# Kernel optimization log

Measured on AMD Instinct MI355X. Metric: run time of the kernel, lower is better.

The kernel has to match this reference:

```python
import jax, jax.numpy as jnp
import numpy as np

H, I_, N, K, R, NL = 768, 1536, 16, 4, 48, 8
B, L, DIN = 4, 1024, 13
DA, RP = 128, 4
EPS = 1e-5

def _rmsnorm(x, w):
    v = jnp.mean(jnp.square(x), axis=-1, keepdims=True)
    return x * jax.lax.rsqrt(v + EPS) * w

def _causal_dwconv(hs, w, b):
    # hs: [B, I, L]; w: [I, K] depthwise kernel; causal (left) padding = K-1
    out = jax.lax.conv_general_dilated(
        hs, w[:, None, :], window_strides=(1,), padding=[(K - 1, 0)],
        dimension_numbers=('NCH', 'OIH', 'NCH'), feature_group_count=hs.shape[1])
    return out + b[None, :, None]

def _selective_scan(u, dt, Bm, Cm, A, D):
    # u, dt: [B, L, I]; Bm, Cm: [B, L, N]; A: [I, N]; D: [I]
    def step(h, inp):
        dt_t, B_t, C_t, u_t = inp          # [B,I], [B,N], [B,N], [B,I]
        dA = jnp.exp(dt_t[:, :, None] * A)  # [B,I,N]
        h = dA * h + (dt_t * u_t)[:, :, None] * B_t[:, None, :]
        y = jnp.einsum('bin,bn->bi', h, C_t)
        return h, y
    h0 = jnp.zeros((u.shape[0], A.shape[0], A.shape[1]), u.dtype)
    xs = (jnp.swapaxes(dt, 0, 1), jnp.swapaxes(Bm, 0, 1),
          jnp.swapaxes(Cm, 0, 1), jnp.swapaxes(u, 0, 1))
    _, ys = jax.lax.scan(step, h0, xs)
    return jnp.swapaxes(ys, 0, 1) + u * D

def _mamba_block(x, norm_w, in_w, conv_w, conv_b, xproj_w, dt_w, dt_b, A_log, D, out_w):
    res = x
    h = _rmsnorm(x, norm_w)
    proj = h @ in_w.T                      # [B,L,2I]
    hs, gate = jnp.split(proj, 2, axis=-1)
    hs = jnp.swapaxes(hs, 1, 2)            # [B,I,L]
    hs = jax.nn.silu(_causal_dwconv(hs, conv_w, conv_b))
    u = jnp.swapaxes(hs, 1, 2)             # [B,L,I]
    ssm = u @ xproj_w.T                    # [B,L,R+2N]
    ts, Bm, Cm = ssm[..., :R], ssm[..., R:R + N], ssm[..., R + N:]
    dt = jax.nn.softplus(ts @ dt_w.T + dt_b)
    y = _selective_scan(u, dt, Bm, Cm, -jnp.exp(A_log), D)
    y = y * jax.nn.silu(gate)
    return res + y @ out_w.T

def _forward(x, mlp_in_w1, mlp_in_b1, mlp_in_w2, mlp_in_b2, mlp_in_w3, mlp_in_b3,
             layers_norm_w, layers_in_proj_w, layers_conv_w, layers_conv_b,
             layers_x_proj_w, layers_dt_w, layers_dt_b, layers_A_log, layers_D,
             layers_out_proj_w, norm_f_w, attn_ws1, attn_ws2,
             mlp_out_w1, mlp_out_b1, mlp_out_w2, mlp_out_b2, mlp_out_w3, mlp_out_b3):
    h = jax.nn.relu(x @ mlp_in_w1.T + mlp_in_b1)
    h = jax.nn.relu(h @ mlp_in_w2.T + mlp_in_b2)
    h = h @ mlp_in_w3.T + mlp_in_b3        # [B,L,H]
    for l in range(NL):
        h = _mamba_block(h, layers_norm_w[l], layers_in_proj_w[l], layers_conv_w[l],
                         layers_conv_b[l], layers_x_proj_w[l], layers_dt_w[l],
                         layers_dt_b[l], layers_A_log[l], layers_D[l],
                         layers_out_proj_w[l])
    h = _rmsnorm(h, norm_f_w)              # final norm_f
    # attention pooling: softmax over the sequence dim (dim=1)
    attn = jax.nn.softmax(jnp.tanh(h @ attn_ws1.T) @ attn_ws2.T, axis=1)  # [B,L,r]
    m = jnp.einsum('blr,blh->brh', attn, h)  # bmm(attn^T, h) -> [B,r,H]
    flat = m.reshape(m.shape[0], -1)         # [B, r*H]
    o = jax.nn.relu(flat @ mlp_out_w1.T + mlp_out_b1)
    o = jax.nn.relu(o @ mlp_out_w2.T + mlp_out_b2)
    return o @ mlp_out_w3.T + mlp_out_b3     # [B,1]

def setup_inputs():
    key = jax.random.key(0)
    ks = iter(jax.random.split(key, 40))
    def nrm(shape, s=0.02):
        return jax.random.normal(next(ks), shape, dtype=jnp.float32) * s
    A_log = jnp.log(jnp.tile(jnp.arange(1, N + 1, dtype=jnp.float32)[None, None, :], (NL, I_, 1)))
    return {
        'x': jax.random.normal(next(ks), (B, L, DIN), dtype=jnp.float32),
        'mlp_in_w1': nrm((256, DIN)), 'mlp_in_b1': jnp.zeros((256,), jnp.float32),
        'mlp_in_w2': nrm((256, 256)), 'mlp_in_b2': jnp.zeros((256,), jnp.float32),
        'mlp_in_w3': nrm((H, 256)), 'mlp_in_b3': jnp.zeros((H,), jnp.float32),
        'layers_norm_w': jnp.ones((NL, H), jnp.float32),
        'layers_in_proj_w': nrm((NL, 2 * I_, H)),
        'layers_conv_w': nrm((NL, I_, K), 0.1),
        'layers_conv_b': jnp.zeros((NL, I_), jnp.float32),
        'layers_x_proj_w': nrm((NL, R + 2 * N, I_)),
        'layers_dt_w': nrm((NL, I_, R)),
        'layers_dt_b': jnp.full((NL, I_), -4.6, jnp.float32),
        'layers_A_log': A_log,
        'layers_D': jnp.ones((NL, I_), jnp.float32),
        'layers_out_proj_w': nrm((NL, H, I_)),
        'norm_f_w': jnp.ones((H,), jnp.float32),
        'attn_ws1': nrm((DA, H)), 'attn_ws2': nrm((RP, DA)),
        'mlp_out_w1': nrm((256, H * RP)), 'mlp_out_b1': jnp.zeros((256,), jnp.float32),
        'mlp_out_w2': nrm((256, 256)), 'mlp_out_b2': jnp.zeros((256,), jnp.float32),
        'mlp_out_w3': nrm((1, 256)), 'mlp_out_b3': jnp.zeros((1,), jnp.float32),
    }

def reference(x, mlp_in_w1, mlp_in_b1, mlp_in_w2, mlp_in_b2, mlp_in_w3, mlp_in_b3,
              layers_norm_w, layers_in_proj_w, layers_conv_w, layers_conv_b,
              layers_x_proj_w, layers_dt_w, layers_dt_b, layers_A_log, layers_D,
              layers_out_proj_w, norm_f_w, attn_ws1, attn_ws2,
              mlp_out_w1, mlp_out_b1, mlp_out_w2, mlp_out_b2, mlp_out_w3, mlp_out_b3):
    return _forward(x, mlp_in_w1, mlp_in_b1, mlp_in_w2, mlp_in_b2, mlp_in_w3, mlp_in_b3,
                    layers_norm_w, layers_in_proj_w, layers_conv_w, layers_conv_b,
                    layers_x_proj_w, layers_dt_w, layers_dt_b, layers_A_log, layers_D,
                    layers_out_proj_w, norm_f_w, attn_ws1, attn_ws2,
                    mlp_out_w1, mlp_out_b1, mlp_out_w2, mlp_out_b2, mlp_out_w3, mlp_out_b3)
```

## Files before the change

### kernel.cpp

```cpp
#include <hip/hip_runtime.h>
#include <cstddef>
#include <cstdint>

#define HD    768
#define ID    1536
#define ND    16
#define KD    4
#define RD    48
#define NLAY  8
#define BB    4
#define LL    1024
#define BL    4096
#define DIN   13
#define DA_   128
#define RP_   4

#define NC    32
#define CS    32

typedef _Float16 f16;
typedef f16 f16x8 __attribute__((ext_vector_type(8)));
typedef float f32x4 __attribute__((ext_vector_type(4)));

__device__ __forceinline__ float softplus_f(float x) {
    return (x > 20.f) ? x : log1pf(expf(x));
}

__device__ __forceinline__ float fast_exp2(float x) {
#if __has_builtin(__builtin_amdgcn_exp2f)
    return __builtin_amdgcn_exp2f(x);
#else
    return exp2f(x);
#endif
}

__global__ __launch_bounds__(256) void cast_f16_k(
    const float* __restrict__ in, f16* __restrict__ out, int n)
{
    int i = (blockIdx.x * 256 + threadIdx.x) * 4;
    if (i + 3 < n) {
        float4 v = *(const float4*)(in + i);
        out[i]     = (f16)v.x;
        out[i + 1] = (f16)v.y;
        out[i + 2] = (f16)v.z;
        out[i + 3] = (f16)v.w;
    } else {
        for (int j = i; j < n; ++j) out[j] = (f16)in[j];
    }
}

__global__ __launch_bounds__(256) void cast_dtw_k(
    const float* __restrict__ in, f16* __restrict__ out)
{
    int idx = blockIdx.x * 256 + threadIdx.x;
    if (idx >= NLAY * ID * 64) return;
    int k = idx & 63, r = idx >> 6;
    out[idx] = (k < RD) ? (f16)in[r * RD + k] : (f16)0.f;
}

__global__ __launch_bounds__(256) void zero_k(float* __restrict__ p, int n)
{
    int i = blockIdx.x * 256 + threadIdx.x;
    if (i < n) p[i] = 0.f;
}

__device__ __forceinline__ void epilogue_store(
    float v, int row, int col, int N,
    const float* __restrict__ res, int ldres,
    float* __restrict__ C, int ldc,
    f16* __restrict__ Cb, int ldcb, int ncb, int act,
    const float* __restrict__ bias)
{
    if (col >= N) return;
    if (bias) v += bias[col];
    if (act == 1) v = fmaxf(v, 0.f);
    else if (act == 2) v = tanhf(v);
    else if (act == 3) v = softplus_f(v);
    if (res) v += res[(size_t)row * ldres + col];
    if (C) C[(size_t)row * ldc + col] = v;
    if (Cb && col < ncb) Cb[(size_t)row * ldcb + col] = (f16)v;
}

__device__ __forceinline__ void async_copy16(const f16* g, f16* l) {
    __builtin_amdgcn_global_load_lds(
        (const __attribute__((address_space(1))) void*)g,
        (__attribute__((address_space(3))) void*)l, 16, 0, 0);
}

__global__ __launch_bounds__(256) void hgemm_k(
    const f16* __restrict__ A, int lda,
    const f16* __restrict__ W, int ldw,
    const float* __restrict__ bias,
    const float* __restrict__ res, int ldres,
    float* __restrict__ C, int ldc,
    f16* __restrict__ Cb, int ldcb, int ncb,
    int M, int N, int K, int act)
{
    __shared__ f16 As[128 * 32];
    __shared__ f16 Bs[128 * 32];
    int tid = threadIdx.x;
    int wave = tid >> 6, lane = tid & 63;
    int m0 = blockIdx.y * 128, n0 = blockIdx.x * 128;

    int wm = wave & 1, wn = wave >> 1;
    int lm = lane & 15;
    int kq = (lane >> 4) * 8;

    int srow = lane >> 2;
    int skc  = (lane & 3) * 8;

    f32x4 acc[4][4] = {};

    for (int k0 = 0; k0 < K; k0 += 32) {
#pragma unroll
        for (int it = 0; it < 2; ++it) {
            int c16 = wave + it * 4;
            int row = c16 * 16 + srow;
            const f16* ga = A + (size_t)(m0 + row) * lda + k0 + skc;
            const f16* gb = W + (size_t)(n0 + row) * ldw + k0 + skc;
            async_copy16(ga, As + c16 * 512);
            async_copy16(gb, Bs + c16 * 512);
        }
        __syncthreads();

        f16x8 af[4], bf[4];
#pragma unroll
        for (int mt = 0; mt < 4; ++mt)
            af[mt] = *(const f16x8*)(As + (wm * 64 + mt * 16 + lm) * 32 + kq);
#pragma unroll
        for (int nt = 0; nt < 4; ++nt)
            bf[nt] = *(const f16x8*)(Bs + (wn * 64 + nt * 16 + lm) * 32 + kq);
#pragma unroll
        for (int mt = 0; mt < 4; ++mt)
#pragma unroll
            for (int nt = 0; nt < 4; ++nt)
                acc[mt][nt] = __builtin_amdgcn_mfma_f32_16x16x32_f16(
                    af[mt], bf[nt], acc[mt][nt], 0, 0, 0);
        __syncthreads();
    }

    int rq = (lane >> 4) * 4;
#pragma unroll
    for (int mt = 0; mt < 4; ++mt)
#pragma unroll
        for (int nt = 0; nt < 4; ++nt) {
            int col = n0 + wn * 64 + nt * 16 + lm;
#pragma unroll
            for (int r = 0; r < 4; ++r) {
                int row = m0 + wm * 64 + mt * 16 + rq + r;
                epilogue_store(acc[mt][nt][r], row, col, N, res, ldres,
                               C, ldc, Cb, ldcb, ncb, act, bias);
            }
        }
}

__global__ __launch_bounds__(256) void hgemm64_k(
    const f16* __restrict__ A, int lda,
    const f16* __restrict__ W, int ldw,
    const float* __restrict__ bias,
    const float* __restrict__ res, int ldres,
    float* __restrict__ C, int ldc,
    f16* __restrict__ Cb, int ldcb, int ncb,
    int M, int N, int K, int act)
{
    __shared__ f16 As[64 * 32];
    __shared__ f16 Bs[64 * 32];
    int tid = threadIdx.x;
    int wave = tid >> 6, lane = tid & 63;
    int m0 = blockIdx.y * 64, n0 = blockIdx.x * 64;

    int wm = wave & 1, wn = wave >> 1;
    int lm = lane & 15;
    int kq = (lane >> 4) * 8;

    int srow = tid >> 2;
    int skc  = (tid & 3) * 8;

    f32x4 acc[2][2] = {};

    for (int k0 = 0; k0 < K; k0 += 32) {
        const f16* ga = A + (size_t)(m0 + srow) * lda + k0 + skc;
        const f16* gb = W + (size_t)(n0 + srow) * ldw + k0 + skc;
        async_copy16(ga, As + wave * 512);
        async_copy16(gb, Bs + wave * 512);
        __syncthreads();

        f16x8 af[2], bf[2];
#pragma unroll
        for (int mt = 0; mt < 2; ++mt)
            af[mt] = *(const f16x8*)(As + (wm * 32 + mt * 16 + lm) * 32 + kq);
#pragma unroll
        for (int nt = 0; nt < 2; ++nt)
            bf[nt] = *(const f16x8*)(Bs + (wn * 32 + nt * 16 + lm) * 32 + kq);
#pragma unroll
        for (int mt = 0; mt < 2; ++mt)
#pragma unroll
            for (int nt = 0; nt < 2; ++nt)
                acc[mt][nt] = __builtin_amdgcn_mfma_f32_16x16x32_f16(
                    af[mt], bf[nt], acc[mt][nt], 0, 0, 0);
        __syncthreads();
    }

    int rq = (lane >> 4) * 4;
#pragma unroll
    for (int mt = 0; mt < 2; ++mt)
#pragma unroll
        for (int nt = 0; nt < 2; ++nt) {
            int col = n0 + wn * 32 + nt * 16 + lm;
#pragma unroll
            for (int r = 0; r < 4; ++r) {
                int row = m0 + wm * 32 + mt * 16 + rq + r;
                epilogue_store(acc[mt][nt][r], row, col, N, res, ldres,
                               C, ldc, Cb, ldcb, ncb, act, bias);
            }
        }
}

#define BM 64
#define BN 64
#define BKK 16
__global__ __launch_bounds__(256) void gemm_k(
    const float* __restrict__ A, int lda,
    const float* __restrict__ W,
    const float* __restrict__ bias,
    float* __restrict__ C, int ldc,
    f16* __restrict__ Cb, int ldcb,
    int M, int N, int K, int act)
{
    __shared__ float As[BKK][BM + 4];
    __shared__ float Ws[BKK][BN + 4];
    int tid = threadIdx.x;
    int tx = tid & 15, ty = tid >> 4;
    int m0 = blockIdx.y * BM, n0 = blockIdx.x * BN;
    float acc[4][4] = {};
    int arow = tid >> 2;
    int acol = (tid & 3) * 4;

    for (int k0 = 0; k0 < K; k0 += BKK) {
        int gm = m0 + arow;
        int gn = n0 + arow;
#pragma unroll
        for (int j = 0; j < 4; ++j) {
            int gk = k0 + acol + j;
            float av = 0.f, wv = 0.f;
            if (gm < M && gk < K) av = A[(size_t)gm * lda + gk];
            if (gn < N && gk < K) wv = W[(size_t)gn * K + gk];
            As[acol + j][arow] = av;
            Ws[acol + j][arow] = wv;
        }
        __syncthreads();
#pragma unroll
        for (int k = 0; k < BKK; ++k) {
            float a[4], b[4];
#pragma unroll
            for (int i = 0; i < 4; ++i) a[i] = As[k][ty * 4 + i];
#pragma unroll
            for (int j = 0; j < 4; ++j) b[j] = Ws[k][tx * 4 + j];
#pragma unroll
            for (int i = 0; i < 4; ++i)
#pragma unroll
                for (int j = 0; j < 4; ++j)
                    acc[i][j] += a[i] * b[j];
        }
        __syncthreads();
    }

#pragma unroll
    for (int i = 0; i < 4; ++i) {
        int row = m0 + ty * 4 + i;
        if (row >= M) continue;
#pragma unroll
        for (int j = 0; j < 4; ++j) {
            int col = n0 + tx * 4 + j;
            if (col >= N) continue;
            float v = acc[i][j];
            if (bias) v += bias[col];
            if (act == 1) v = fmaxf(v, 0.f);
            if (C) C[(size_t)row * ldc + col] = v;
            if (Cb) Cb[(size_t)row * ldcb + col] = (f16)v;
        }
    }
}

__global__ __launch_bounds__(256) void rmsnorm_k(
    const float* __restrict__ x, const float* __restrict__ w,
    f16* __restrict__ out)
{
    int row = blockIdx.x;
    const float* xr = x + (size_t)row * HD;
    int tid = threadIdx.x;
    float v0 = xr[tid], v1 = xr[tid + 256], v2 = xr[tid + 512];
    __shared__ float red[256];
    red[tid] = v0 * v0 + v1 * v1 + v2 * v2;
    __syncthreads();
    for (int o = 128; o; o >>= 1) {
        if (tid < o) red[tid] += red[tid + o];
        __syncthreads();
    }
    float scale = rsqrtf(red[0] / (float)HD + 1e-5f);
    f16* outr = out + (size_t)row * HD;
    outr[tid]       = (f16)(v0 * scale * w[tid]);
    outr[tid + 256] = (f16)(v1 * scale * w[tid + 256]);
    outr[tid + 512] = (f16)(v2 * scale * w[tid + 512]);
}

__global__ __launch_bounds__(256) void conv_silu_k(
    const f16* __restrict__ projb, const float* __restrict__ cw,
    const float* __restrict__ cb, f16* __restrict__ ub)
{
    int idx = blockIdx.x * 256 + threadIdx.x;
    if (idx >= BL * (ID / 8)) return;
    int i8  = (idx % (ID / 8)) * 8;
    int row = idx / (ID / 8);
    int t = row & (LL - 1);

    float4 wv[8];
#pragma unroll
    for (int j = 0; j < 8; ++j)
        wv[j] = *(const float4*)(cw + (i8 + j) * KD);

    float s[8];
    float4 cb0 = *(const float4*)(cb + i8);
    float4 cb1 = *(const float4*)(cb + i8 + 4);
    s[0] = cb0.x; s[1] = cb0.y; s[2] = cb0.z; s[3] = cb0.w;
    s[4] = cb1.x; s[5] = cb1.y; s[6] = cb1.z; s[7] = cb1.w;

#pragma unroll
    for (int k = 0; k < KD; ++k) {
        int tt = t - (KD - 1) + k;
        if (tt < 0) continue;
        f16x8 p = *(const f16x8*)(projb + (size_t)(row - (KD - 1) + k) * (2 * ID) + i8);
#pragma unroll
        for (int j = 0; j < 8; ++j) {
            float wk = (k == 0) ? wv[j].x : (k == 1) ? wv[j].y
                     : (k == 2) ? wv[j].z : wv[j].w;
            s[j] += (float)p[j] * wk;
        }
    }
    f16x8 o;
#pragma unroll
    for (int j = 0; j < 8; ++j) {
        float v = s[j] / (1.f + expf(-s[j]));
        o[j] = (f16)v;
    }
    *(f16x8*)(ub + (size_t)row * ID + i8) = o;
}

__global__ __launch_bounds__(256) void scan1_k(
    const f16*   __restrict__ dtf,
    const float* __restrict__ ssm,
    const f16*   __restrict__ ub,
    const float* __restrict__ A_log,
    float* __restrict__ Pw, float* __restrict__ Hw)
{
    int b = blockIdx.z, c = blockIdx.y;
    int i = blockIdx.x * 256 + threadIdx.x;
    __shared__ float sB[CS * 16];
    for (int idx = threadIdx.x; idx < CS * 16; idx += 256) {
        int t = idx >> 4, n = idx & 15;
        sB[idx] = ssm[((size_t)(b * LL + c * CS + t)) * 80 + 48 + n];
    }
    __syncthreads();

    float Ain[16];
#pragma unroll
    for (int n = 0; n < 16; ++n)
        Ain[n] = -expf(A_log[i * ND + n]) * 1.44269504f;

    float h[16];
    float sdt = 0.f;
#pragma unroll
    for (int n = 0; n < 16; ++n) h[n] = 0.f;

    for (int t = 0; t < CS; ++t) {
        size_t row = (size_t)(b * LL + c * CS + t);
        float dtv = (float)dtf[row * ID + i];
        float x = dtv * (float)ub[row * ID + i];
        sdt += dtv;
        const float4* Bv = (const float4*)(sB + t * 16);
        float4 B0 = Bv[0], B1 = Bv[1], B2 = Bv[2], B3 = Bv[3];
        float Bf[16] = {B0.x, B0.y, B0.z, B0.w, B1.x, B1.y, B1.z, B1.w,
                        B2.x, B2.y, B2.z, B2.w, B3.x, B3.y, B3.z, B3.w};
#pragma unroll
        for (int n = 0; n < 16; ++n) {
            float dA = fast_exp2(dtv * Ain[n]);
            h[n] = dA * h[n] + x * Bf[n];
        }
    }
    size_t off = (((size_t)(b * NC + c) * ID + i) << 4);
    float4* pw = (float4*)(Pw + off);
    float4* hw = (float4*)(Hw + off);
#pragma unroll
    for (int q = 0; q < 4; ++q) {
        pw[q] = make_float4(fast_exp2(sdt * Ain[q*4]),
                            fast_exp2(sdt * Ain[q*4+1]),
                            fast_exp2(sdt * Ain[q*4+2]),
                            fast_exp2(sdt * Ain[q*4+3]));
        hw[q] = make_float4(h[q*4], h[q*4+1], h[q*4+2], h[q*4+3]);
    }
}

__global__ __launch_bounds__(256) void scan_comb_k(
    const float* __restrict__ Pw, float* __restrict__ Hw)
{
    int idx = blockIdx.x * 256 + threadIdx.x;
    int rem = idx & (ID * 16 - 1);
    int b = idx / (ID * 16);
    size_t base = (size_t)b * NC * ID * 16 + rem;
    float e = 0.f;
    for (int c = 0; c < NC; ++c) {
        size_t off = base + (size_t)c * ID * 16;
        float Hc = Hw[off];
        float Pc = Pw[off];
        Hw[off] = e;
        e = Hc + Pc * e;
    }
}

__global__ __launch_bounds__(256) void scan2_k(
    const f16*   __restrict__ dtf,
    const float* __restrict__ ssm,
    const f16*   __restrict__ ub,
    const f16*   __restrict__ projb,
    const float* __restrict__ A_log,
    const float* __restrict__ D,
    const float* __restrict__ Hw,
    f16* __restrict__ y)
{
    int b = blockIdx.z, c = blockIdx.y;
    int i = blockIdx.x * 256 + threadIdx.x;
    __shared__ float sB[CS * 16];
    __shared__ float sC[CS * 16];
    for (int idx = threadIdx.x; idx < CS * 16; idx += 256) {
        int t = idx >> 4, n = idx & 15;
        size_t row = (size_t)(b * LL + c * CS + t);
        sB[idx] = ssm[row * 80 + 48 + n];
        sC[idx] = ssm[row * 80 + 64 + n];
    }
    __syncthreads();

    float Ain[16];
#pragma unroll
    for (int n = 0; n < 16; ++n)
        Ain[n] = -expf(A_log[i * ND + n]) * 1.44269504f;
    float Dv = D[i];

    float h[16];
    size_t off = (((size_t)(b * NC + c) * ID + i) << 4);
    const float4* hw = (const float4*)(Hw + off);
#pragma unroll
    for (int q = 0; q < 4; ++q) {
        float4 v = hw[q];
        h[q*4] = v.x; h[q*4+1] = v.y; h[q*4+2] = v.z; h[q*4+3] = v.w;
    }

    for (int t = 0; t < CS; ++t) {
        size_t row = (size_t)(b * LL + c * CS + t);
        float dtv = (float)dtf[row * ID + i];
        float uv  = (float)ub[row * ID + i];
        float g   = (float)projb[row * (2 * ID) + ID + i];
        float x = dtv * uv;
        const float4* Bv = (const float4*)(sB + t * 16);
        const float4* Cv = (const float4*)(sC + t * 16);
        float4 B0 = Bv[0], B1 = Bv[1], B2 = Bv[2], B3 = Bv[3];
        float4 C0 = Cv[0], C1 = Cv[1], C2 = Cv[2], C3 = Cv[3];
        float Bf[16] = {B0.x, B0.y, B0.z, B0.w, B1.x, B1.y, B1.z, B1.w,
                        B2.x, B2.y, B2.z, B2.w, B3.x, B3.y, B3.z, B3.w};
        float Cf[16] = {C0.x, C0.y, C0.z, C0.w, C1.x, C1.y, C1.z, C1.w,
                        C2.x, C2.y, C2.z, C2.w, C3.x, C3.y, C3.z, C3.w};
        float yv = 0.f;
#pragma unroll
        for (int n = 0; n < 16; ++n) {
            float dA = fast_exp2(dtv * Ain[n]);
            h[n] = dA * h[n] + x * Bf[n];
            yv += h[n] * Cf[n];
        }
        yv = (yv + uv * Dv) * (g / (1.f + expf(-g)));
        y[row * ID + i] = (f16)yv;
    }
}

__global__ __launch_bounds__(256) void softmax_k(
    const float* __restrict__ s, float* __restrict__ attn)
{
    int b = blockIdx.x >> 2, r = blockIdx.x & 3;
    int tid = threadIdx.x;
    __shared__ float red[256];
    float mx = -1e30f;
    for (int j = 0; j < 4; ++j) {
        int t = tid + j * 256;
        mx = fmaxf(mx, s[((size_t)(b * LL + t)) * RP_ + r]);
    }
    red[tid] = mx;
    __syncthreads();
    for (int o = 128; o; o >>= 1) {
        if (tid < o) red[tid] = fmaxf(red[tid], red[tid + o]);
        __syncthreads();
    }
    mx = red[0];
    __syncthreads();
    float ev[4], sum = 0.f;
    for (int j = 0; j < 4; ++j) {
        int t = tid + j * 256;
        ev[j] = expf(s[((size_t)(b * LL + t)) * RP_ + r] - mx);
        sum += ev[j];
    }
    red[tid] = sum;
    __syncthreads();
    for (int o = 128; o; o >>= 1) {
        if (tid < o) red[tid] += red[tid + o];
        __syncthreads();
    }
    float inv = 1.f / red[0];
    for (int j = 0; j < 4; ++j) {
        int t = tid + j * 256;
        attn[((size_t)(b * LL + t)) * RP_ + r] = ev[j] * inv;
    }
}

__global__ __launch_bounds__(256) void pool_k(
    const float* __restrict__ attn, const f16* __restrict__ hn,
    float* __restrict__ m)
{
    int br = blockIdx.x;
    int b = br >> 2, r = br & 3;
    int t0 = blockIdx.y * 64;
    int tid = threadIdx.x;
    float acc0 = 0.f, acc1 = 0.f, acc2 = 0.f;
    for (int t = t0; t < t0 + 64; ++t) {
        float w = attn[((size_t)(b * LL + t)) * RP_ + r];
        const f16* hr = hn + ((size_t)(b * LL + t)) * HD;
        acc0 += w * (float)hr[tid];
        acc1 += w * (float)hr[tid + 256];
        acc2 += w * (float)hr[tid + 512];
    }
    float* outp = m + ((size_t)(b * RP_ + r)) * HD;
    atomicAdd(outp + tid, acc0);
    atomicAdd(outp + tid + 256, acc1);
    atomicAdd(outp + tid + 512, acc2);
}

__global__ __launch_bounds__(64) void gemv_k(
    const float* __restrict__ A, int lda,
    const float* __restrict__ W, const float* __restrict__ bias,
    float* __restrict__ C, int ldc, int K, int relu)
{
    int n = blockIdx.x, b = blockIdx.y;
    int lane = threadIdx.x;
    const float* a = A + (size_t)b * lda;
    const float* w = W + (size_t)n * K;
    float s = 0.f;
    for (int k = lane; k < K; k += 64) s += a[k] * w[k];
    for (int off = 32; off; off >>= 1) s += __shfl_down(s, off);
    if (lane == 0) {
        float v = s + (bias ? bias[n] : 0.f);
        if (relu) v = fmaxf(v, 0.f);
        C[(size_t)b * ldc + n] = v;
    }
}

extern "C" void kernel_launch(void* const* d_in, const int* in_sizes, int n_in,
                              void* d_out, int out_size, void* d_ws, size_t ws_size,
                              hipStream_t stream) {
    const float* x          = (const float*)d_in[0];
    const float* mlp_in_w1  = (const float*)d_in[1];
    const float* mlp_in_b1  = (const float*)d_in[2];
    const float* mlp_in_w2  = (const float*)d_in[3];
    const float* mlp_in_b2  = (const float*)d_in[4];
    const float* mlp_in_w3  = (const float*)d_in[5];
    const float* mlp_in_b3  = (const float*)d_in[6];
    const float* norm_w     = (const float*)d_in[7];
    const float* in_proj_w  = (const float*)d_in[8];
    const float* conv_w     = (const float*)d_in[9];
    const float* conv_b     = (const float*)d_in[10];
    const float* x_proj_w   = (const float*)d_in[11];
    const float* dt_w       = (const float*)d_in[12];
    const float* dt_b       = (const float*)d_in[13];
    const float* A_log      = (const float*)d_in[14];
    const float* Dp         = (const float*)d_in[15];
    const float* out_proj_w = (const float*)d_in[16];
    const float* norm_f_w   = (const float*)d_in[17];
    const float* attn_ws1   = (const float*)d_in[18];
    const float* attn_ws2   = (const float*)d_in[19];
    const float* mlp_out_w1 = (const float*)d_in[20];
    const float* mlp_out_b1 = (const float*)d_in[21];
    const float* mlp_out_w2 = (const float*)d_in[22];
    const float* mlp_out_b2 = (const float*)d_in[23];
    const float* mlp_out_w3 = (const float*)d_in[24];
    const float* mlp_out_b3 = (const float*)d_in[25];
    float* out = (float*)d_out;

    float* ws   = (float*)d_ws;
    float* h    = ws;
    float* ssm  = h    + (size_t)BL * HD;
    float* h1a  = ssm  + (size_t)BL * 80;
    float* sbuf = h1a  + (size_t)BL * DA_;
    float* attn = sbuf + (size_t)BL * 4;
    float* mbuf = attn + (size_t)BL * 4;
    float* o1   = mbuf + (size_t)BB * RP_ * HD;
    float* o2   = o1   + (size_t)BB * 256;
    float* Pw   = o2   + (size_t)BB * 256;
    float* Hw   = Pw   + (size_t)BB * NC * ID * 16;
    f16* fb    = (f16*)(Hw + (size_t)BB * NC * ID * 16);
    f16* h1b   = fb;
    f16* h2b   = h1b  + (size_t)BL * 256;
    f16* hnb   = h2b  + (size_t)BL * 256;
    f16* projb = hnb  + (size_t)BL * HD;
    f16* ub    = projb+ (size_t)BL * 2 * ID;
    f16* ssmb  = ub   + (size_t)BL * ID;
    f16* dtf   = ssmb + (size_t)BL * 64;
    f16* ybb   = dtf  + (size_t)BL * ID;
    f16* opwf  = ybb  + (size_t)BL * ID;
    f16* xpwf  = opwf + (size_t)NLAY * HD * ID;
    f16* dwwf  = xpwf + (size_t)NLAY * 80 * ID;
    f16* w2f   = dwwf + (size_t)NLAY * ID * 64;
    f16* w3f   = w2f  + 256 * 256;
    f16* a1f   = w3f  + HD * 256;
    f16* ipwf  = a1f  + DA_ * HD;

    size_t used_bytes = (size_t)((char*)(ipwf) - (char*)d_ws);
    size_t slot_bytes = (size_t)2 * ID * HD * sizeof(f16);
    int full = (ws_size >= used_bytes + (size_t)NLAY * slot_bytes) ? 1 : 0;

    dim3 blk(256);
    auto cgrid = [](int n) { return dim3((n / 4 + 255) / 256); };

    cast_f16_k<<<cgrid(256 * 256), blk, 0, stream>>>(mlp_in_w2, w2f, 256 * 256);
    cast_f16_k<<<cgrid(HD * 256), blk, 0, stream>>>(mlp_in_w3, w3f, HD * 256);
    cast_f16_k<<<cgrid(DA_ * HD), blk, 0, stream>>>(attn_ws1, a1f, DA_ * HD);
    cast_f16_k<<<cgrid(NLAY * HD * ID), blk, 0, stream>>>(out_proj_w, opwf, NLAY * HD * ID);
    cast_f16_k<<<cgrid(NLAY * 80 * ID), blk, 0, stream>>>(x_proj_w, xpwf, NLAY * 80 * ID);
    cast_dtw_k<<<(NLAY * ID * 64 + 255) / 256, blk, 0, stream>>>(dt_w, dwwf);
    if (full)
        cast_f16_k<<<cgrid(NLAY * 2 * ID * HD), blk, 0, stream>>>(
            in_proj_w, ipwf, NLAY * 2 * ID * HD);

    gemm_k<<<dim3(4, 64), blk, 0, stream>>>(
        x, DIN, mlp_in_w1, mlp_in_b1, nullptr, 0, h1b, 256, BL, 256, DIN, 1);
    hgemm64_k<<<dim3(4, 64), blk, 0, stream>>>(
        h1b, 256, w2f, 256, mlp_in_b2, nullptr, 0, nullptr, 0, h2b, 256, 256,
        BL, 256, 256, 1);
    hgemm64_k<<<dim3(12, 64), blk, 0, stream>>>(
        h2b, 256, w3f, 256, mlp_in_b3, nullptr, 0, h, HD, nullptr, 0, 0,
        BL, HD, 256, 0);

    for (int l = 0; l < NLAY; ++l) {
        const float* nw  = norm_w + (size_t)l * HD;
        const float* cw  = conv_w + (size_t)l * ID * KD;
        const float* cb  = conv_b + (size_t)l * ID;
        const float* db  = dt_b   + (size_t)l * ID;
        const float* al  = A_log  + (size_t)l * ID * ND;
        const float* dv  = Dp     + (size_t)l * ID;

        const f16* ipw;
        if (full) {
            ipw = ipwf + (size_t)l * 2 * ID * HD;
        } else {
            cast_f16_k<<<cgrid(2 * ID * HD), blk, 0, stream>>>(
                in_proj_w + (size_t)l * 2 * ID * HD, ipwf, 2 * ID * HD);
            ipw = ipwf;
        }
        rmsnorm_k<<<BL, blk, 0, stream>>>(h, nw, hnb);
        hgemm_k<<<dim3(24, 32), blk, 0, stream>>>(
            hnb, HD, ipw, HD, nullptr, nullptr, 0, nullptr, 0,
            projb, 2 * ID, 2 * ID, BL, 2 * ID, HD, 0);
        conv_silu_k<<<(BL * (ID / 8) + 255) / 256, blk, 0, stream>>>(
            projb, cw, cb, ub);
        hgemm64_k<<<dim3(2, 64), blk, 0, stream>>>(
            ub, ID, xpwf + (size_t)l * 80 * ID, ID, nullptr, nullptr, 0,
            ssm, 80, ssmb, 64, RD, BL, 80, ID, 0);
        hgemm64_k<<<dim3(24, 64), blk, 0, stream>>>(
            ssmb, 64, dwwf + (size_t)l * ID * 64, 64, db, nullptr, 0,
            nullptr, 0, dtf, ID, ID, BL, ID, 64, 3);

        scan1_k<<<dim3(ID / 256, NC, BB), blk, 0, stream>>>(
            dtf, ssm, ub, al, Pw, Hw);
        scan_comb_k<<<(BB * ID * 16) / 256, blk, 0, stream>>>(Pw, Hw);
        scan2_k<<<dim3(ID / 256, NC, BB), blk, 0, stream>>>(
            dtf, ssm, ub, projb, al, dv, Hw, ybb);

        hgemm64_k<<<dim3(12, 64), blk, 0, stream>>>(
            ybb, ID, opwf + (size_t)l * HD * ID, ID, nullptr, h, HD,
            h, HD, nullptr, 0, 0, BL, HD, ID, 0);
    }

    rmsnorm_k<<<BL, blk, 0, stream>>>(h, norm_f_w, hnb);
    hgemm64_k<<<dim3(2, 64), blk, 0, stream>>>(
        hnb, HD, a1f, HD, nullptr, nullptr, 0, h1a, DA_, nullptr, 0, 0,
        BL, DA_, HD, 2);
    gemm_k<<<dim3(1, 64), blk, 0, stream>>>(
        h1a, DA_, attn_ws2, nullptr, sbuf, RP_, nullptr, 0, BL, RP_, DA_, 0);
    softmax_k<<<BB * RP_, blk, 0, stream>>>(sbuf, attn);
    zero_k<<<(BB * RP_ * HD + 255) / 256, blk, 0, stream>>>(mbuf, BB * RP_ * HD);
    pool_k<<<dim3(BB * RP_, LL / 64), blk, 0, stream>>>(attn, hnb, mbuf);

    gemv_k<<<dim3(256, BB), dim3(64), 0, stream>>>(
        mbuf, RP_ * HD, mlp_out_w1, mlp_out_b1, o1, 256, RP_ * HD, 1);
    gemv_k<<<dim3(256, BB), dim3(64), 0, stream>>>(
        o1, 256, mlp_out_w2, mlp_out_b2, o2, 256, 256, 1);
    gemv_k<<<dim3(1, BB), dim3(64), 0, stream>>>(
        o2, 256, mlp_out_w3, mlp_out_b3, out, 1, 256, 0);
}
```

Before: 2.182 ms.

## Double GEMM K-tile to 64 and split-K the x_proj GEMM

Both f16 MFMA GEMM kernels now stage 64-wide K slices per iteration instead of 32, halving the number of barrier pairs and loop iterations per K. The x_proj GEMM (N=80, only 128 blocks) is replaced by a 4-way split-K kernel writing partials, followed by a combine kernel that sums them, writes ssm and the padded f16 copy. This aims to fix low occupancy on the skinny GEMM at the cost of extra partial-buffer traffic, one more launch, and doubled LDS per block.

```diff
diff --git a/kernel.cpp b/kernel.cpp
--- a/kernel.cpp
+++ b/kernel.cpp
@@ -96,8 +96,8 @@
     f16* __restrict__ Cb, int ldcb, int ncb,
     int M, int N, int K, int act)
 {
-    __shared__ f16 As[128 * 32];
-    __shared__ f16 Bs[128 * 32];
+    __shared__ f16 As[128 * 64];
+    __shared__ f16 Bs[128 * 64];
     int tid = threadIdx.x;
     int wave = tid >> 6, lane = tid & 63;
     int m0 = blockIdx.y * 128, n0 = blockIdx.x * 128;
@@ -106,36 +106,42 @@
     int lm = lane & 15;
     int kq = (lane >> 4) * 8;
 
-    int srow = lane >> 2;
-    int skc  = (lane & 3) * 8;
+    int srow = tid >> 2;
+    int skc  = (tid & 3) * 8;
 
     f32x4 acc[4][4] = {};
 
-    for (int k0 = 0; k0 < K; k0 += 32) {
-#pragma unroll
-        for (int it = 0; it < 2; ++it) {
-            int c16 = wave + it * 4;
-            int row = c16 * 16 + srow;
-            const f16* ga = A + (size_t)(m0 + row) * lda + k0 + skc;
-            const f16* gb = W + (size_t)(n0 + row) * ldw + k0 + skc;
-            async_copy16(ga, As + c16 * 512);
-            async_copy16(gb, Bs + c16 * 512);
-        }
-        __syncthreads();
-
-        f16x8 af[4], bf[4];
-#pragma unroll
-        for (int mt = 0; mt < 4; ++mt)
-            af[mt] = *(const f16x8*)(As + (wm * 64 + mt * 16 + lm) * 32 + kq);
-#pragma unroll
-        for (int nt = 0; nt < 4; ++nt)
-            bf[nt] = *(const f16x8*)(Bs + (wn * 64 + nt * 16 + lm) * 32 + kq);
-#pragma unroll
-        for (int mt = 0; mt < 4; ++mt)
+    for (int k0 = 0; k0 < K; k0 += 64) {
+#pragma unroll
+        for (int it = 0; it < 4; ++it) {
+            int rowo = (it & 1) * 64 + srow;
+            int kk   = (it >> 1) * 32 + skc;
+            int base = (it >> 1) * 4096 + (it & 1) * 2048 + wave * 512;
+            async_copy16(A + (size_t)(m0 + rowo) * lda + k0 + kk, As + base);
+            async_copy16(W + (size_t)(n0 + rowo) * ldw + k0 + kk, Bs + base);
+        }
+        __syncthreads();
+
+        f16x8 af[4][2], bf[4][2];
+#pragma unroll
+        for (int ks = 0; ks < 2; ++ks) {
+#pragma unroll
+            for (int mt = 0; mt < 4; ++mt)
+                af[mt][ks] = *(const f16x8*)(As + ks * 4096 +
+                                 (wm * 64 + mt * 16 + lm) * 32 + kq);
 #pragma unroll
             for (int nt = 0; nt < 4; ++nt)
-                acc[mt][nt] = __builtin_amdgcn_mfma_f32_16x16x32_f16(
-                    af[mt], bf[nt], acc[mt][nt], 0, 0, 0);
+                bf[nt][ks] = *(const f16x8*)(Bs + ks * 4096 +
+                                 (wn * 64 + nt * 16 + lm) * 32 + kq);
+        }
+#pragma unroll
+        for (int ks = 0; ks < 2; ++ks)
+#pragma unroll
+            for (int mt = 0; mt < 4; ++mt)
+#pragma unroll
+                for (int nt = 0; nt < 4; ++nt)
+                    acc[mt][nt] = __builtin_amdgcn_mfma_f32_16x16x32_f16(
+                        af[mt][ks], bf[nt][ks], acc[mt][nt], 0, 0, 0);
         __syncthreads();
     }
 
@@ -163,8 +169,8 @@
     f16* __restrict__ Cb, int ldcb, int ncb,
     int M, int N, int K, int act)
 {
-    __shared__ f16 As[64 * 32];
-    __shared__ f16 Bs[64 * 32];
+    __shared__ f16 As[64 * 64];
+    __shared__ f16 Bs[64 * 64];
     int tid = threadIdx.x;
     int wave = tid >> 6, lane = tid & 63;
     int m0 = blockIdx.y * 64, n0 = blockIdx.x * 64;
@@ -178,26 +184,36 @@
 
     f32x4 acc[2][2] = {};
 
-    for (int k0 = 0; k0 < K; k0 += 32) {
-        const f16* ga = A + (size_t)(m0 + srow) * lda + k0 + skc;
-        const f16* gb = W + (size_t)(n0 + srow) * ldw + k0 + skc;
-        async_copy16(ga, As + wave * 512);
-        async_copy16(gb, Bs + wave * 512);
-        __syncthreads();
-
-        f16x8 af[2], bf[2];
-#pragma unroll
-        for (int mt = 0; mt < 2; ++mt)
-            af[mt] = *(const f16x8*)(As + (wm * 32 + mt * 16 + lm) * 32 + kq);
-#pragma unroll
-        for (int nt = 0; nt < 2; ++nt)
-            bf[nt] = *(const f16x8*)(Bs + (wn * 32 + nt * 16 + lm) * 32 + kq);
-#pragma unroll
-        for (int mt = 0; mt < 2; ++mt)
+    for (int k0 = 0; k0 < K; k0 += 64) {
+#pragma unroll
+        for (int it = 0; it < 2; ++it) {
+            int kk   = it * 32 + skc;
+            int base = it * 2048 + wave * 512;
+            async_copy16(A + (size_t)(m0 + srow) * lda + k0 + kk, As + base);
+            async_copy16(W + (size_t)(n0 + srow) * ldw + k0 + kk, Bs + base);
+        }
+        __syncthreads();
+
+        f16x8 af[2][2], bf[2][2];
+#pragma unroll
+        for (int ks = 0; ks < 2; ++ks) {
+#pragma unroll
+            for (int mt = 0; mt < 2; ++mt)
+                af[mt][ks] = *(const f16x8*)(As + ks * 2048 +
+                                 (wm * 32 + mt * 16 + lm) * 32 + kq);
 #pragma unroll
             for (int nt = 0; nt < 2; ++nt)
-                acc[mt][nt] = __builtin_amdgcn_mfma_f32_16x16x32_f16(
-                    af[mt], bf[nt], acc[mt][nt], 0, 0, 0);
+                bf[nt][ks] = *(const f16x8*)(Bs + ks * 2048 +
+                                 (wn * 32 + nt * 16 + lm) * 32 + kq);
+        }
+#pragma unroll
+        for (int ks = 0; ks < 2; ++ks)
+#pragma unroll
+            for (int mt = 0; mt < 2; ++mt)
+#pragma unroll
+                for (int nt = 0; nt < 2; ++nt)
+                    acc[mt][nt] = __builtin_amdgcn_mfma_f32_16x16x32_f16(
+                        af[mt][ks], bf[nt][ks], acc[mt][nt], 0, 0, 0);
         __syncthreads();
     }
 
@@ -214,6 +230,95 @@
                                C, ldc, Cb, ldcb, ncb, act, bias);
             }
         }
+}
+
+__global__ __launch_bounds__(256) void hgemm64s_k(
+    const f16* __restrict__ A, int lda,
+    const f16* __restrict__ W, int ldw,
+    float* __restrict__ Cp, int ldc, size_t PS,
+    int N, int kPer)
+{
+    __shared__ f16 As[64 * 64];
+    __shared__ f16 Bs[64 * 64];
+    int tid = threadIdx.x;
+    int wave = tid >> 6, lane = tid & 63;
+    int m0 = blockIdx.y * 64, n0 = blockIdx.x * 64;
+    int z = blockIdx.z;
+    int kbeg = z * kPer, kend = kbeg + kPer;
+
+    int wm = wave & 1, wn = wave >> 1;
+    int lm = lane & 15;
+    int kq = (lane >> 4) * 8;
+    int srow = tid >> 2;
+    int skc  = (tid & 3) * 8;
+
+    f32x4 acc[2][2] = {};
+
+    for (int k0 = kbeg; k0 < kend; k0 += 64) {
+#pragma unroll
+        for (int it = 0; it < 2; ++it) {
+            int kk   = it * 32 + skc;
+            int base = it * 2048 + wave * 512;
+            async_copy16(A + (size_t)(m0 + srow) * lda + k0 + kk, As + base);
+            async_copy16(W + (size_t)(n0 + srow) * ldw + k0 + kk, Bs + base);
+        }
+        __syncthreads();
+
+        f16x8 af[2][2], bf[2][2];
+#pragma unroll
+        for (int ks = 0; ks < 2; ++ks) {
+#pragma unroll
+            for (int mt = 0; mt < 2; ++mt)
+                af[mt][ks] = *(const f16x8*)(As + ks * 2048 +
+                                 (wm * 32 + mt * 16 + lm) * 32 + kq);
+#pragma unroll
+            for (int nt = 0; nt < 2; ++nt)
+                bf[nt][ks] = *(const f16x8*)(Bs + ks * 2048 +
+                                 (wn * 32 + nt * 16 + lm) * 32 + kq);
+        }
+#pragma unroll
+        for (int ks = 0; ks < 2; ++ks)
+#pragma unroll
+            for (int mt = 0; mt < 2; ++mt)
+#pragma unroll
+                for (int nt = 0; nt < 2; ++nt)
+                    acc[mt][nt] = __builtin_amdgcn_mfma_f32_16x16x32_f16(
+                        af[mt][ks], bf[nt][ks], acc[mt][nt], 0, 0, 0);
+        __syncthreads();
+    }
+
+    float* C = Cp + (size_t)z * PS;
+    int rq = (lane >> 4) * 4;
+#pragma unroll
+    for (int mt = 0; mt < 2; ++mt)
+#pragma unroll
+        for (int nt = 0; nt < 2; ++nt) {
+            int col = n0 + wn * 32 + nt * 16 + lm;
+            if (col >= N) continue;
+#pragma unroll
+            for (int r = 0; r < 4; ++r) {
+                int row = m0 + wm * 32 + mt * 16 + rq + r;
+                C[(size_t)row * ldc + col] = acc[mt][nt][r];
+            }
+        }
+}
+
+__global__ __launch_bounds__(256) void xcomb_k(
+    const float* __restrict__ part, float* __restrict__ ssm,
+    f16* __restrict__ ssmb)
+{
+    int idx = blockIdx.x * 256 + threadIdx.x;
+    if (idx >= BL * 96) return;
+    int row = idx / 96, c = idx % 96;
+    const size_t PS = (size_t)BL * 80;
+    if (c < 80) {
+        size_t o = (size_t)row * 80 + c;
+        float s = part[o] + part[PS + o] + part[2 * PS + o] + part[3 * PS + o];
+        ssm[o] = s;
+        if (c < RD) ssmb[(size_t)row * 64 + c] = (f16)s;
+    } else {
+        ssmb[(size_t)row * 64 + (c - 80 + RD)] = (f16)0.f;
+    }
 }
 
 #define BM 64
@@ -590,17 +695,18 @@
     const float* mlp_out_b3 = (const float*)d_in[25];
     float* out = (float*)d_out;
 
-    float* ws   = (float*)d_ws;
-    float* h    = ws;
-    float* ssm  = h    + (size_t)BL * HD;
-    float* h1a  = ssm  + (size_t)BL * 80;
-    float* sbuf = h1a  + (size_t)BL * DA_;
-    float* attn = sbuf + (size_t)BL * 4;
-    float* mbuf = attn + (size_t)BL * 4;
-    float* o1   = mbuf + (size_t)BB * RP_ * HD;
-    float* o2   = o1   + (size_t)BB * 256;
-    float* Pw   = o2   + (size_t)BB * 256;
-    float* Hw   = Pw   + (size_t)BB * NC * ID * 16;
+    float* ws    = (float*)d_ws;
+    float* h     = ws;
+    float* ssm   = h    + (size_t)BL * HD;
+    float* xpart = ssm  + (size_t)BL * 80;
+    float* h1a   = xpart+ (size_t)4 * BL * 80;
+    float* sbuf  = h1a  + (size_t)BL * DA_;
+    float* attn  = sbuf + (size_t)BL * 4;
+    float* mbuf  = attn + (size_t)BL * 4;
+    float* o1    = mbuf + (size_t)BB * RP_ * HD;
+    float* o2    = o1   + (size_t)BB * 256;
+    float* Pw    = o2   + (size_t)BB * 256;
+    float* Hw    = Pw   + (size_t)BB * NC * ID * 16;
     f16* fb    = (f16*)(Hw + (size_t)BB * NC * ID * 16);
     f16* h1b   = fb;
     f16* h2b   = h1b  + (size_t)BL * 256;
@@ -666,9 +772,12 @@
             projb, 2 * ID, 2 * ID, BL, 2 * ID, HD, 0);
         conv_silu_k<<<(BL * (ID / 8) + 255) / 256, blk, 0, stream>>>(
             projb, cw, cb, ub);
-        hgemm64_k<<<dim3(2, 64), blk, 0, stream>>>(
-            ub, ID, xpwf + (size_t)l * 80 * ID, ID, nullptr, nullptr, 0,
-            ssm, 80, ssmb, 64, RD, BL, 80, ID, 0);
+
+        hgemm64s_k<<<dim3(2, 64, 4), blk, 0, stream>>>(
+            ub, ID, xpwf + (size_t)l * 80 * ID, ID,
+            xpart, 80, (size_t)BL * 80, 80, ID / 4);
+        xcomb_k<<<(BL * 96 + 255) / 256, blk, 0, stream>>>(xpart, ssm, ssmb);
+
         hgemm64_k<<<dim3(24, 64), blk, 0, stream>>>(
             ssmb, 64, dwwf + (size_t)l * ID * 64, 64, db, nullptr, 0,
             nullptr, 0, dtf, ID, ID, BL, ID, 64, 3);
```

New measurement: 2.247 ms. 3.0% more time.
